# Performance work log

Measured on AMD Instinct MI355X. Metric: run time of the kernel, lower is better.

The kernel has to match this reference:

```python
import jax, jax.numpy as jnp
import numpy as np

T, B, F = 256, 256, 128      # time, batch, features
H, L, K = 384, 3, 10         # hidden_dim, levels, conv_size
C = H // L                   # chunk_size = 128
G = 4 * H + 2 * L            # gate projection width = 1542
S = H // 6                   # scale bottleneck = 64


def setup_inputs() -> dict:
    key = jax.random.key(0)
    ks = jax.random.split(key, 14)
    s = 0.02
    n = lambda k, shp: (jax.random.normal(k, shp, jnp.float32) * s)
    return {
        "x":   jax.random.normal(ks[0], (T, B, F), jnp.float32),
        "Wk":  n(ks[1], (F + 1, G)),   # input kernel (in+interval -> 4H+2L)
        "bk":  jnp.zeros((G,), jnp.float32),
        "Wr":  n(ks[2], (H + 1, G)),   # recurrent kernel
        "br":  jnp.zeros((G,), jnp.float32),
        "Ws":  n(ks[3], (H, S)),       # nn_scale
        "bs":  jnp.zeros((S,), jnp.float32),
        "Wrs": n(ks[4], (S, H)),       # nn_rescale
        "brs": jnp.zeros((H,), jnp.float32),
        "Wc":  n(ks[5], (H, H, K)),    # nn_conv weight (out, in, kernel)
        "bc":  jnp.zeros((H,), jnp.float32),
        "Wo":  n(ks[6], (H, 1)),       # nn_output (n_class==2 -> out_dim 1)
        "bo":  jnp.zeros((1,), jnp.float32),
    }


def _forward(x, Wk, bk, Wr, br, Ws, bs, Wrs, brs, Wc, bc, Wo, bo):
    Bs = x.shape[1]
    ones = jnp.ones((Bs, 1), x.dtype)

    def step(carry, x_t):
        c, h, buf_h, buf_d = carry
        xo = (jnp.concatenate([x_t, ones], -1) @ Wk + bk
              + jnp.concatenate([h, ones], -1) @ Wr + br)       # (B, G)
        # hierarchical master gates (ON-LSTM cumax)
        fm = jnp.cumsum(jax.nn.softmax(xo[:, :L], -1), -1)       # l2r (B,L)
        im = jnp.flip(jnp.cumsum(jax.nn.softmax(
            jnp.flip(xo[:, L:2 * L], -1), -1), -1), -1)          # r2l (B,L)
        g = xo[:, 2 * L:].reshape(Bs, 4 * L, C)
        f_g = jax.nn.sigmoid(g[:, :L])
        i_g = jax.nn.sigmoid(g[:, L:2 * L])
        o_g = jax.nn.sigmoid(g[:, 2 * L:3 * L])
        c_in = jnp.tanh(g[:, 3 * L:])
        c_l = c.reshape(Bs, L, C)
        fm3, im3 = fm[:, :, None], im[:, :, None]
        ov = fm3 * im3
        c_new = ov * (f_g * c_l + i_g * c_in) + (fm3 - ov) * c_l + (im3 - ov) * c_in
        h_new = (o_g * jnp.tanh(c_new)).reshape(Bs, H)
        c_new = c_new.reshape(Bs, H)
        cur_d = 1.0 - jnp.mean(fm, -1)                           # (B,)
        # sliding window buffers (K, B, H) / (K, B)
        buf_h = jnp.concatenate([buf_h[1:], h_new[None]], 0)
        buf_d = jnp.concatenate([buf_d[1:], cur_d[None]], 0)
        local_dis = jax.nn.softmax(jnp.cumsum(buf_d.T, 1), 1)    # (B, K)
        local_h = buf_h.transpose(1, 2, 0) * local_dis[:, None, :]  # (B,H,K)
        theme = jax.nn.sigmoid(
            jax.nn.relu(jnp.mean(local_h, -1) @ Ws + bs) @ Wrs + brs)  # (B,H)
        conv = jnp.einsum('bik,oik->bo', local_h, Wc) + bc      # window conv1d
        loc = theme * conv
        return (c_new, h_new, buf_h, buf_d), (h_new, loc)

    init = (jnp.zeros((Bs, H), x.dtype), jnp.zeros((Bs, H), x.dtype),
            jnp.zeros((K, Bs, H), x.dtype), jnp.zeros((K, Bs), x.dtype))
    _, (h_all, loc_all) = jax.lax.scan(step, init, x)
    # residual add, output head, keep last timestep only (as original)
    rnn_last = loc_all[-1] + h_all[-1]                           # (B, H)
    out = jax.nn.sigmoid(rnn_last @ Wo + bo)                     # (B, 1)
    return out


def reference(x, Wk, bk, Wr, br, Ws, bs, Wrs, brs, Wc, bc, Wo, bo):
    return _forward(x, Wk, bk, Wr, br, Ws, bs, Wrs, brs, Wc, bc, Wo, bo)
```

## Files before the change

kernel.cpp:

```cpp
#include <hip/hip_runtime.h>
#include <hip/hip_bf16.h>
#include <math.h>

#define T_STEPS 256
#define BATCH   256
#define FDIM    128
#define HDIM    384
#define LLEV    3
#define KWIN    10
#define GDIM    1542
#define SDIM    64
#define NPAD    1600
#define KA      512
#define BH      (BATCH*HDIM)

typedef __bf16 bf16x8 __attribute__((ext_vector_type(8)));
typedef float  f32x4  __attribute__((ext_vector_type(4)));

__device__ __forceinline__ float sigmoidf_(float x){ return 1.f/(1.f+__expf(-x)); }

__global__ void init_state(float* __restrict__ hf, float* __restrict__ c, __bf16* __restrict__ hb){
    int i = blockIdx.x*256 + threadIdx.x;
    hf[i] = 0.f; c[i] = 0.f; hb[i] = (__bf16)0.f;
}

__global__ void cast_x(const float* __restrict__ x, __bf16* __restrict__ xb, int n){
    int i = (blockIdx.x*256 + threadIdx.x)*4;
    if (i < n){
        float4 v = *(const float4*)(x+i);
        xb[i+0]=(__bf16)v.x; xb[i+1]=(__bf16)v.y; xb[i+2]=(__bf16)v.z; xb[i+3]=(__bf16)v.w;
    }
}

__global__ void pack_w(const float* __restrict__ Wk, const float* __restrict__ bk,
                       const float* __restrict__ Wr, const float* __restrict__ br,
                       __bf16* __restrict__ Bp, float* __restrict__ cvec){
    int gid = blockIdx.x*256 + threadIdx.x;
    int k8  = gid / NPAD;
    int col = gid - k8*NPAD;
    bool valid = (col < 6) || (col >= 64);
    int g = (col < 6) ? col : (col - 58);
    bf16x8 out;
    #pragma unroll
    for (int j=0;j<8;++j){
        int k = k8*8 + j;
        float v = 0.f;
        if (valid) v = (k < HDIM) ? Wr[k*GDIM + g] : Wk[(k-HDIM)*GDIM + g];
        out[j] = (__bf16)v;
    }
    *(bf16x8*)(Bp + (size_t)gid*8) = out;
    if (k8 == 0){
        float cv = 0.f;
        if (valid) cv = Wk[FDIM*GDIM + g] + bk[g] + Wr[HDIM*GDIM + g] + br[g];
        cvec[col] = cv;
    }
}

__global__ __launch_bounds__(256) void step_gemm(const __bf16* __restrict__ hb, const __bf16* __restrict__ xb,
                                                 const __bf16* __restrict__ Bp, const float* __restrict__ cvec,
                                                 float* __restrict__ xo, int t){
    int wave = threadIdx.x >> 6;
    int lane = threadIdx.x & 63;
    int nblk = blockIdx.x % 25;
    int mblk = blockIdx.x / 25;
    int m0 = mblk*64 + wave*16;
    int n0 = nblk*64;
    int row = m0 + (lane & 15);
    int kh  = (lane >> 4) * 8;
    f32x4 acc[4] = {};
    const __bf16* hrow = hb + (size_t)row*HDIM;
    const __bf16* xrow = xb + ((size_t)t*BATCH + row)*FDIM;
    #pragma unroll
    for (int ks=0; ks<12; ++ks){
        int k = ks*32 + kh;
        bf16x8 a = *(const bf16x8*)(hrow + k);
        const __bf16* bp = Bp + (((size_t)(k>>3))*NPAD + n0 + (lane & 15))*8;
        #pragma unroll
        for (int nt=0; nt<4; ++nt){
            bf16x8 bfrag = *(const bf16x8*)(bp + nt*16*8);
            acc[nt] = __builtin_amdgcn_mfma_f32_16x16x32_bf16(a, bfrag, acc[nt], 0,0,0);
        }
    }
    #pragma unroll
    for (int ks=12; ks<16; ++ks){
        int k = ks*32 + kh;
        bf16x8 a = *(const bf16x8*)(xrow + (k - HDIM));
        const __bf16* bp = Bp + (((size_t)(k>>3))*NPAD + n0 + (lane & 15))*8;
        #pragma unroll
        for (int nt=0; nt<4; ++nt){
            bf16x8 bfrag = *(const bf16x8*)(bp + nt*16*8);
            acc[nt] = __builtin_amdgcn_mfma_f32_16x16x32_bf16(a, bfrag, acc[nt], 0,0,0);
        }
    }
    int r0   = m0 + ((lane >> 4) << 2);
    int ccol = lane & 15;
    #pragma unroll
    for (int nt=0; nt<4; ++nt){
        int col = n0 + nt*16 + ccol;
        float cv = cvec[col];
        #pragma unroll
        for (int i=0;i<4;++i)
            xo[(size_t)(r0+i)*NPAD + col] = acc[nt][i] + cv;
    }
}

__global__ void step_gates(const float* __restrict__ xo, float* __restrict__ c,
                           float* __restrict__ hf, __bf16* __restrict__ hb,
                           float* __restrict__ bufh, float* __restrict__ bufd, int t){
    int gid = blockIdx.x*256 + threadIdx.x;
    int b = gid / HDIM;
    int u = gid - b*HDIM;
    const float* xr = xo + (size_t)b*NPAD;
    float a0=xr[0], a1=xr[1], a2=xr[2];
    float m1 = fmaxf(fmaxf(a0,a1),a2);
    float e0=__expf(a0-m1), e1=__expf(a1-m1), e2=__expf(a2-m1);
    float inv = 1.f/(e0+e1+e2);
    float fm0 = e0*inv, fm1 = fm0 + e1*inv, fm2 = fm1 + e2*inv;
    float b0=xr[3], b1=xr[4], b2=xr[5];
    float m2 = fmaxf(fmaxf(b0,b1),b2);
    float f0=__expf(b0-m2), f1=__expf(b1-m2), f2=__expf(b2-m2);
    float inv2 = 1.f/(f0+f1+f2);
    float im2 = f2*inv2, im1 = im2 + f1*inv2, im0 = im1 + f0*inv2;
    int l = u >> 7;
    float fml = (l==0)?fm0:((l==1)?fm1:fm2);
    float iml = (l==0)?im0:((l==1)?im1:im2);
    float fg = sigmoidf_(xr[64 + u]);
    float ig = sigmoidf_(xr[64 + 384 + u]);
    float og = sigmoidf_(xr[64 + 768 + u]);
    float ci = tanhf   (xr[64 + 1152 + u]);
    float cold = c[gid];
    float ov = fml*iml;
    float cn = ov*(fg*cold + ig*ci) + (fml-ov)*cold + (iml-ov)*ci;
    float h  = og * tanhf(cn);
    c[gid] = cn; hf[gid] = h; hb[gid] = (__bf16)h;
    if (t >= T_STEPS - KWIN){
        int slot = t - (T_STEPS - KWIN);
        bufh[(size_t)slot*BH + gid] = h;
        if (u == 0) bufd[slot*BATCH + b] = 1.f - (fm0+fm1+fm2)*(1.f/3.f);
    }
}

__global__ void final_locdis(const float* __restrict__ bufd, float* __restrict__ locdis){
    int b = threadIdx.x;
    float d[KWIN]; float cum = 0.f;
    #pragma unroll
    for (int k=0;k<KWIN;++k){ cum += bufd[k*BATCH + b]; d[k] = cum; }
    float m = d[0];
    #pragma unroll
    for (int k=1;k<KWIN;++k) m = fmaxf(m, d[k]);
    float s = 0.f;
    #pragma unroll
    for (int k=0;k<KWIN;++k){ d[k] = __expf(d[k]-m); s += d[k]; }
    float invs = 1.f/s;
    #pragma unroll
    for (int k=0;k<KWIN;++k) locdis[b*KWIN + k] = d[k]*invs;
}

__global__ void final_lh(const float* __restrict__ bufh, const float* __restrict__ locdis,
                         float* __restrict__ lh, float* __restrict__ mh){
    int gid = blockIdx.x*256 + threadIdx.x;
    int b = gid / HDIM;
    int i = gid - b*HDIM;
    float s = 0.f;
    #pragma unroll
    for (int k=0;k<KWIN;++k){
        float v = bufh[(size_t)k*BH + gid] * locdis[b*KWIN + k];
        lh[(size_t)b*(HDIM*KWIN) + i*KWIN + k] = v;
        s += v;
    }
    mh[gid] = s * (1.f/KWIN);
}

__global__ __launch_bounds__(256) void final_conv(const float* __restrict__ lh, const float* __restrict__ Wc,
                                                  const float* __restrict__ bc, float* __restrict__ cvout){
    __shared__ float As[32*257];
    __shared__ float Bs[32*257];
    int tid = threadIdx.x;
    int bb = blockIdx.x / 12, ob = blockIdx.x % 12;
    int tx = tid & 15, ty = tid >> 4;
    float acc00=0.f, acc01=0.f, acc10=0.f, acc11=0.f;
    const int KD = HDIM*KWIN;
    for (int ch=0; ch<15; ++ch){
        #pragma unroll
        for (int p=0;p<8;++p){
            int q   = tid + p*256;
            int row = q >> 6;
            int c4  = q & 63;
            float4 va = *(const float4*)(lh + (size_t)(bb*32+row)*KD + ch*256 + c4*4);
            float4 vb = *(const float4*)(Wc + (size_t)(ob*32+row)*KD + ch*256 + c4*4);
            int o = row*257 + c4*4;
            As[o+0]=va.x; As[o+1]=va.y; As[o+2]=va.z; As[o+3]=va.w;
            Bs[o+0]=vb.x; Bs[o+1]=vb.y; Bs[o+2]=vb.z; Bs[o+3]=vb.w;
        }
        __syncthreads();
        for (int kk=0; kk<256; ++kk){
            float x0 = As[ty*257+kk],      x1 = As[(ty+16)*257+kk];
            float w0 = Bs[tx*257+kk],      w1 = Bs[(tx+16)*257+kk];
            acc00 += x0*w0; acc01 += x0*w1; acc10 += x1*w0; acc11 += x1*w1;
        }
        __syncthreads();
    }
    int r0 = bb*32+ty, r1 = r0+16, o0 = ob*32+tx, o1 = o0+16;
    cvout[(size_t)r0*HDIM + o0] = acc00 + bc[o0];
    cvout[(size_t)r0*HDIM + o1] = acc01 + bc[o1];
    cvout[(size_t)r1*HDIM + o0] = acc10 + bc[o0];
    cvout[(size_t)r1*HDIM + o1] = acc11 + bc[o1];
}

__global__ void final_th1(const float* __restrict__ mh, const float* __restrict__ Ws,
                          const float* __restrict__ bs, float* __restrict__ th1){
    int gid = blockIdx.x*256 + threadIdx.x;
    int b = gid >> 6, s = gid & 63;
    float acc = bs[s];
    const float* mr = mh + (size_t)b*HDIM;
    for (int i=0;i<HDIM;++i) acc += mr[i] * Ws[i*SDIM + s];
    th1[gid] = fmaxf(acc, 0.f);
}

__global__ void final_theme(const float* __restrict__ th1, const float* __restrict__ Wrs,
                            const float* __restrict__ brs, float* __restrict__ theme){
    int gid = blockIdx.x*256 + threadIdx.x;
    int b = gid / HDIM, o = gid - b*HDIM;
    float acc = brs[o];
    const float* tr = th1 + b*SDIM;
    for (int j=0;j<SDIM;++j) acc += tr[j] * Wrs[j*HDIM + o];
    theme[gid] = sigmoidf_(acc);
}

__global__ void final_out(const float* __restrict__ theme, const float* __restrict__ cvout,
                          const float* __restrict__ hf, const float* __restrict__ Wo,
                          const float* __restrict__ bo, float* __restrict__ out){
    int b = blockIdx.x, lane = threadIdx.x;
    float s = 0.f;
    for (int u=lane; u<HDIM; u+=64){
        float r = theme[(size_t)b*HDIM+u]*cvout[(size_t)b*HDIM+u] + hf[(size_t)b*HDIM+u];
        s += r * Wo[u];
    }
    #pragma unroll
    for (int off=32; off; off>>=1) s += __shfl_down(s, off);
    if (lane == 0) out[b] = sigmoidf_(s + bo[0]);
}

extern "C" void kernel_launch(void* const* d_in, const int* in_sizes, int n_in,
                              void* d_out, int out_size, void* d_ws, size_t ws_size,
                              hipStream_t stream){
    const float* x   = (const float*)d_in[0];
    const float* Wk  = (const float*)d_in[1];
    const float* bk  = (const float*)d_in[2];
    const float* Wr  = (const float*)d_in[3];
    const float* br  = (const float*)d_in[4];
    const float* Ws  = (const float*)d_in[5];
    const float* bs  = (const float*)d_in[6];
    const float* Wrs = (const float*)d_in[7];
    const float* brs = (const float*)d_in[8];
    const float* Wc  = (const float*)d_in[9];
    const float* bc  = (const float*)d_in[10];
    const float* Wo  = (const float*)d_in[11];
    const float* bo  = (const float*)d_in[12];
    float* out = (float*)d_out;

    char* w = (char*)d_ws;
    auto alloc = [&](size_t bytes)->char*{ char* p = w; w += (bytes + 255) & ~(size_t)255; return p; };
    __bf16* xb    = (__bf16*)alloc((size_t)T_STEPS*BATCH*FDIM*2);
    __bf16* Bp    = (__bf16*)alloc((size_t)(KA/8)*NPAD*8*2);
    float* cvec   = (float*) alloc(NPAD*4);
    float* hf     = (float*) alloc((size_t)BH*4);
    __bf16* hb    = (__bf16*)alloc((size_t)BH*2);
    float* c      = (float*) alloc((size_t)BH*4);
    float* xo     = (float*) alloc((size_t)BATCH*NPAD*4);
    float* bufh   = (float*) alloc((size_t)KWIN*BH*4);
    float* bufd   = (float*) alloc((size_t)KWIN*BATCH*4);
    float* locdis = (float*) alloc((size_t)BATCH*KWIN*4);
    float* lh     = (float*) alloc((size_t)BATCH*HDIM*KWIN*4);
    float* mh     = (float*) alloc((size_t)BH*4);
    float* th1    = (float*) alloc((size_t)BATCH*SDIM*4);
    float* theme  = (float*) alloc((size_t)BH*4);
    float* convb  = (float*) alloc((size_t)BH*4);

    init_state<<<dim3(BH/256), dim3(256), 0, stream>>>(hf, c, hb);
    cast_x<<<dim3((T_STEPS*BATCH*FDIM)/4/256), dim3(256), 0, stream>>>(x, xb, T_STEPS*BATCH*FDIM);
    pack_w<<<dim3((KA/8)*NPAD/256), dim3(256), 0, stream>>>(Wk, bk, Wr, br, Bp, cvec);

    for (int t=0; t<T_STEPS; ++t){
        step_gemm <<<dim3(100), dim3(256), 0, stream>>>(hb, xb, Bp, cvec, xo, t);
        step_gates<<<dim3(BH/256), dim3(256), 0, stream>>>(xo, c, hf, hb, bufh, bufd, t);
    }

    final_locdis<<<dim3(1),   dim3(256), 0, stream>>>(bufd, locdis);
    final_lh    <<<dim3(BH/256), dim3(256), 0, stream>>>(bufh, locdis, lh, mh);
    final_conv  <<<dim3(96),  dim3(256), 0, stream>>>(lh, Wc, bc, convb);
    final_th1   <<<dim3(BATCH*SDIM/256), dim3(256), 0, stream>>>(mh, Ws, bs, th1);
    final_theme <<<dim3(BH/256), dim3(256), 0, stream>>>(th1, Wrs, brs, theme);
    final_out   <<<dim3(BATCH), dim3(64), 0, stream>>>(theme, convb, hf, Wo, bo, out);
}
```

Baseline: 2.410 ms.

## Fuse per-step gate GEMM with LSTM cell update using gate-interleaved weight layout

Merges the per-timestep GEMM and gate-activation kernels into one kernel. The gate weights are repacked so each block's 64 output columns hold the f/i/o/c gates for the same 16 hidden units, and the 6 master-gate columns are computed redundantly by every block through an extra MFMA. The cell update then runs directly from registers, and the hidden state is ping-ponged between two buffers. This removes one launch per step and the global round trip of the xo intermediate, at the cost of duplicated head MFMAs and a block-wide sync.

```diff
diff --git a/kernel.cpp b/kernel.cpp
--- a/kernel.cpp
+++ b/kernel.cpp
@@ -10,7 +10,7 @@
 #define KWIN    10
 #define GDIM    1542
 #define SDIM    64
-#define NPAD    1600
+#define NGC     1536
 #define KA      512
 #define BH      (BATCH*HDIM)
 
@@ -19,9 +19,9 @@
 
 __device__ __forceinline__ float sigmoidf_(float x){ return 1.f/(1.f+__expf(-x)); }
 
-__global__ void init_state(float* __restrict__ hf, float* __restrict__ c, __bf16* __restrict__ hb){
+__global__ void init_state(float* __restrict__ c, __bf16* __restrict__ hbA){
     int i = blockIdx.x*256 + threadIdx.x;
-    hf[i] = 0.f; c[i] = 0.f; hb[i] = (__bf16)0.f;
+    c[i] = 0.f; hbA[i] = (__bf16)0.f;
 }
 
 __global__ void cast_x(const float* __restrict__ x, __bf16* __restrict__ xb, int n){
@@ -32,111 +32,135 @@
     }
 }
 
-__global__ void pack_w(const float* __restrict__ Wk, const float* __restrict__ bk,
-                       const float* __restrict__ Wr, const float* __restrict__ br,
-                       __bf16* __restrict__ Bp, float* __restrict__ cvec){
-    int gid = blockIdx.x*256 + threadIdx.x;
-    int k8  = gid / NPAD;
-    int col = gid - k8*NPAD;
-    bool valid = (col < 6) || (col >= 64);
-    int g = (col < 6) ? col : (col - 58);
+__global__ void pack_w_gate(const float* __restrict__ Wk, const float* __restrict__ bk,
+                            const float* __restrict__ Wr, const float* __restrict__ br,
+                            __bf16* __restrict__ Bg, float* __restrict__ cg){
+    int gid = blockIdx.x*256 + threadIdx.x;
+    int k8  = gid / NGC;
+    int col = gid - k8*NGC;
+    int ugrp = col >> 6;
+    int rem  = col & 63;
+    int gate = rem >> 4;
+    int um   = rem & 15;
+    int u    = ugrp*16 + um;
+    int g    = 6 + gate*HDIM + u;
+    bf16x8 out;
+    #pragma unroll
+    for (int j=0;j<8;++j){
+        int k = k8*8 + j;
+        float v = (k < HDIM) ? Wr[k*GDIM + g] : Wk[(k-HDIM)*GDIM + g];
+        out[j] = (__bf16)v;
+    }
+    *(bf16x8*)(Bg + (size_t)gid*8) = out;
+    if (k8 == 0)
+        cg[col] = Wk[FDIM*GDIM + g] + bk[g] + Wr[HDIM*GDIM + g] + br[g];
+}
+
+__global__ void pack_w_head(const float* __restrict__ Wk, const float* __restrict__ bk,
+                            const float* __restrict__ Wr, const float* __restrict__ br,
+                            __bf16* __restrict__ Bh, float* __restrict__ ch){
+    int gid = blockIdx.x*256 + threadIdx.x;
+    int k8  = gid >> 4;
+    int colh = gid & 15;
     bf16x8 out;
     #pragma unroll
     for (int j=0;j<8;++j){
         int k = k8*8 + j;
         float v = 0.f;
-        if (valid) v = (k < HDIM) ? Wr[k*GDIM + g] : Wk[(k-HDIM)*GDIM + g];
+        if (colh < 6) v = (k < HDIM) ? Wr[k*GDIM + colh] : Wk[(k-HDIM)*GDIM + colh];
         out[j] = (__bf16)v;
     }
-    *(bf16x8*)(Bp + (size_t)gid*8) = out;
-    if (k8 == 0){
-        float cv = 0.f;
-        if (valid) cv = Wk[FDIM*GDIM + g] + bk[g] + Wr[HDIM*GDIM + g] + br[g];
-        cvec[col] = cv;
-    }
-}
-
-__global__ __launch_bounds__(256) void step_gemm(const __bf16* __restrict__ hb, const __bf16* __restrict__ xb,
-                                                 const __bf16* __restrict__ Bp, const float* __restrict__ cvec,
-                                                 float* __restrict__ xo, int t){
-    int wave = threadIdx.x >> 6;
-    int lane = threadIdx.x & 63;
-    int nblk = blockIdx.x % 25;
-    int mblk = blockIdx.x / 25;
-    int m0 = mblk*64 + wave*16;
-    int n0 = nblk*64;
-    int row = m0 + (lane & 15);
-    int kh  = (lane >> 4) * 8;
-    f32x4 acc[4] = {};
-    const __bf16* hrow = hb + (size_t)row*HDIM;
-    const __bf16* xrow = xb + ((size_t)t*BATCH + row)*FDIM;
-    #pragma unroll
-    for (int ks=0; ks<12; ++ks){
+    *(bf16x8*)(Bh + (size_t)gid*8) = out;
+    if (k8 == 0)
+        ch[colh] = (colh < 6) ? (Wk[FDIM*GDIM + colh] + bk[colh] + Wr[HDIM*GDIM + colh] + br[colh]) : 0.f;
+}
+
+__global__ __launch_bounds__(256) void step_fused(
+    const __bf16* __restrict__ hbp, __bf16* __restrict__ hbn,
+    const __bf16* __restrict__ xb,
+    const __bf16* __restrict__ Bg, const __bf16* __restrict__ Bh,
+    const float* __restrict__ cg, const float* __restrict__ ch,
+    float* __restrict__ c, float* __restrict__ hf,
+    float* __restrict__ bufh, float* __restrict__ bufd, int t)
+{
+    __shared__ float headlds[4][16][8];
+    int tid  = threadIdx.x;
+    int wave = tid >> 6, lane = tid & 63;
+    int mblk = blockIdx.x / 24, ublk = blockIdx.x % 24;
+    int m0   = mblk*64 + wave*16;
+    int ccol = lane & 15;
+    int krow = lane >> 4;
+    int arow = m0 + ccol;
+    int kh   = krow*8;
+
+    f32x4 acc[4] = {}; f32x4 acch = {};
+    const __bf16* hrow   = hbp + (size_t)arow*HDIM;
+    const __bf16* xrow   = xb + ((size_t)t*BATCH + arow)*FDIM;
+    const __bf16* bgbase = Bg + ((size_t)ublk*64 + ccol)*8;
+    const __bf16* bhbase = Bh + (size_t)ccol*8;
+
+    #pragma unroll
+    for (int ks=0; ks<16; ++ks){
         int k = ks*32 + kh;
-        bf16x8 a = *(const bf16x8*)(hrow + k);
-        const __bf16* bp = Bp + (((size_t)(k>>3))*NPAD + n0 + (lane & 15))*8;
+        bf16x8 a = (ks < 12) ? *(const bf16x8*)(hrow + k)
+                             : *(const bf16x8*)(xrow + (k - HDIM));
+        const __bf16* bp = bgbase + (size_t)(k>>3)*NGC*8;
         #pragma unroll
         for (int nt=0; nt<4; ++nt){
             bf16x8 bfrag = *(const bf16x8*)(bp + nt*16*8);
             acc[nt] = __builtin_amdgcn_mfma_f32_16x16x32_bf16(a, bfrag, acc[nt], 0,0,0);
         }
-    }
-    #pragma unroll
-    for (int ks=12; ks<16; ++ks){
-        int k = ks*32 + kh;
-        bf16x8 a = *(const bf16x8*)(xrow + (k - HDIM));
-        const __bf16* bp = Bp + (((size_t)(k>>3))*NPAD + n0 + (lane & 15))*8;
-        #pragma unroll
-        for (int nt=0; nt<4; ++nt){
-            bf16x8 bfrag = *(const bf16x8*)(bp + nt*16*8);
-            acc[nt] = __builtin_amdgcn_mfma_f32_16x16x32_bf16(a, bfrag, acc[nt], 0,0,0);
-        }
-    }
-    int r0   = m0 + ((lane >> 4) << 2);
-    int ccol = lane & 15;
-    #pragma unroll
-    for (int nt=0; nt<4; ++nt){
-        int col = n0 + nt*16 + ccol;
-        float cv = cvec[col];
+        bf16x8 bh = *(const bf16x8*)(bhbase + (size_t)(k>>3)*16*8);
+        acch = __builtin_amdgcn_mfma_f32_16x16x32_bf16(a, bh, acch, 0,0,0);
+    }
+
+    if (ccol < 6){
+        float cv = ch[ccol];
         #pragma unroll
         for (int i=0;i<4;++i)
-            xo[(size_t)(r0+i)*NPAD + col] = acc[nt][i] + cv;
-    }
-}
-
-__global__ void step_gates(const float* __restrict__ xo, float* __restrict__ c,
-                           float* __restrict__ hf, __bf16* __restrict__ hb,
-                           float* __restrict__ bufh, float* __restrict__ bufd, int t){
-    int gid = blockIdx.x*256 + threadIdx.x;
-    int b = gid / HDIM;
-    int u = gid - b*HDIM;
-    const float* xr = xo + (size_t)b*NPAD;
-    float a0=xr[0], a1=xr[1], a2=xr[2];
-    float m1 = fmaxf(fmaxf(a0,a1),a2);
-    float e0=__expf(a0-m1), e1=__expf(a1-m1), e2=__expf(a2-m1);
-    float inv = 1.f/(e0+e1+e2);
-    float fm0 = e0*inv, fm1 = fm0 + e1*inv, fm2 = fm1 + e2*inv;
-    float b0=xr[3], b1=xr[4], b2=xr[5];
-    float m2 = fmaxf(fmaxf(b0,b1),b2);
-    float f0=__expf(b0-m2), f1=__expf(b1-m2), f2=__expf(b2-m2);
-    float inv2 = 1.f/(f0+f1+f2);
-    float im2 = f2*inv2, im1 = im2 + f1*inv2, im0 = im1 + f0*inv2;
+            headlds[wave][krow*4+i][ccol] = acch[i] + cv;
+    }
+    __syncthreads();
+
+    int u = ublk*16 + ccol;
     int l = u >> 7;
-    float fml = (l==0)?fm0:((l==1)?fm1:fm2);
-    float iml = (l==0)?im0:((l==1)?im1:im2);
-    float fg = sigmoidf_(xr[64 + u]);
-    float ig = sigmoidf_(xr[64 + 384 + u]);
-    float og = sigmoidf_(xr[64 + 768 + u]);
-    float ci = tanhf   (xr[64 + 1152 + u]);
-    float cold = c[gid];
-    float ov = fml*iml;
-    float cn = ov*(fg*cold + ig*ci) + (fml-ov)*cold + (iml-ov)*ci;
-    float h  = og * tanhf(cn);
-    c[gid] = cn; hf[gid] = h; hb[gid] = (__bf16)h;
-    if (t >= T_STEPS - KWIN){
-        int slot = t - (T_STEPS - KWIN);
-        bufh[(size_t)slot*BH + gid] = h;
-        if (u == 0) bufd[slot*BATCH + b] = 1.f - (fm0+fm1+fm2)*(1.f/3.f);
+    float cgv0 = cg[ublk*64 +  0 + ccol];
+    float cgv1 = cg[ublk*64 + 16 + ccol];
+    float cgv2 = cg[ublk*64 + 32 + ccol];
+    float cgv3 = cg[ublk*64 + 48 + ccol];
+    int slot = t - (T_STEPS - KWIN);
+
+    #pragma unroll
+    for (int i=0;i<4;++i){
+        int rl = krow*4 + i;
+        int R  = m0 + rl;
+        float a0 = headlds[wave][rl][0], a1 = headlds[wave][rl][1], a2 = headlds[wave][rl][2];
+        float b0 = headlds[wave][rl][3], b1 = headlds[wave][rl][4], b2 = headlds[wave][rl][5];
+        float m1v = fmaxf(fmaxf(a0,a1),a2);
+        float e0=__expf(a0-m1v), e1=__expf(a1-m1v), e2=__expf(a2-m1v);
+        float inv = 1.f/(e0+e1+e2);
+        float fm0 = e0*inv, fm1 = fm0 + e1*inv, fm2 = fm1 + e2*inv;
+        float m2v = fmaxf(fmaxf(b0,b1),b2);
+        float f0=__expf(b0-m2v), f1=__expf(b1-m2v), f2=__expf(b2-m2v);
+        float inv2 = 1.f/(f0+f1+f2);
+        float im2 = f2*inv2, im1 = im2 + f1*inv2, im0 = im1 + f0*inv2;
+        float fml = (l==0)?fm0:((l==1)?fm1:fm2);
+        float iml = (l==0)?im0:((l==1)?im1:im2);
+        float fg = sigmoidf_(acc[0][i] + cgv0);
+        float ig = sigmoidf_(acc[1][i] + cgv1);
+        float og = sigmoidf_(acc[2][i] + cgv2);
+        float ci = tanhf   (acc[3][i] + cgv3);
+        size_t idx = (size_t)R*HDIM + u;
+        float cold = c[idx];
+        float ov = fml*iml;
+        float cn = ov*(fg*cold + ig*ci) + (fml-ov)*cold + (iml-ov)*ci;
+        float h  = og * tanhf(cn);
+        c[idx] = cn;
+        hbn[idx] = (__bf16)h;
+        if (slot >= 0) bufh[(size_t)slot*BH + idx] = h;
+        if (t == T_STEPS-1) hf[idx] = h;
+        if (slot >= 0 && ublk == 0 && ccol == 0)
+            bufd[slot*BATCH + R] = 1.f - (fm0+fm1+fm2)*(1.f/3.f);
     }
 }
 
@@ -262,12 +286,14 @@
     char* w = (char*)d_ws;
     auto alloc = [&](size_t bytes)->char*{ char* p = w; w += (bytes + 255) & ~(size_t)255; return p; };
     __bf16* xb    = (__bf16*)alloc((size_t)T_STEPS*BATCH*FDIM*2);
-    __bf16* Bp    = (__bf16*)alloc((size_t)(KA/8)*NPAD*8*2);
-    float* cvec   = (float*) alloc(NPAD*4);
+    __bf16* Bg    = (__bf16*)alloc((size_t)(KA/8)*NGC*8*2);
+    __bf16* Bh    = (__bf16*)alloc((size_t)(KA/8)*16*8*2);
+    float* cg     = (float*) alloc(NGC*4);
+    float* ch     = (float*) alloc(16*4);
+    __bf16* hbA   = (__bf16*)alloc((size_t)BH*2);
+    __bf16* hbB   = (__bf16*)alloc((size_t)BH*2);
     float* hf     = (float*) alloc((size_t)BH*4);
-    __bf16* hb    = (__bf16*)alloc((size_t)BH*2);
     float* c      = (float*) alloc((size_t)BH*4);
-    float* xo     = (float*) alloc((size_t)BATCH*NPAD*4);
     float* bufh   = (float*) alloc((size_t)KWIN*BH*4);
     float* bufd   = (float*) alloc((size_t)KWIN*BATCH*4);
     float* locdis = (float*) alloc((size_t)BATCH*KWIN*4);
@@ -277,13 +303,16 @@
     float* theme  = (float*) alloc((size_t)BH*4);
     float* convb  = (float*) alloc((size_t)BH*4);
 
-    init_state<<<dim3(BH/256), dim3(256), 0, stream>>>(hf, c, hb);
+    init_state<<<dim3(BH/256), dim3(256), 0, stream>>>(c, hbA);
     cast_x<<<dim3((T_STEPS*BATCH*FDIM)/4/256), dim3(256), 0, stream>>>(x, xb, T_STEPS*BATCH*FDIM);
-    pack_w<<<dim3((KA/8)*NPAD/256), dim3(256), 0, stream>>>(Wk, bk, Wr, br, Bp, cvec);
+    pack_w_gate<<<dim3((KA/8)*NGC/256), dim3(256), 0, stream>>>(Wk, bk, Wr, br, Bg, cg);
+    pack_w_head<<<dim3((KA/8)*16/256), dim3(256), 0, stream>>>(Wk, bk, Wr, br, Bh, ch);
 
     for (int t=0; t<T_STEPS; ++t){
-        step_gemm <<<dim3(100), dim3(256), 0, stream>>>(hb, xb, Bp, cvec, xo, t);
-        step_gates<<<dim3(BH/256), dim3(256), 0, stream>>>(xo, c, hf, hb, bufh, bufd, t);
+        const __bf16* hp = (t & 1) ? hbB : hbA;
+        __bf16*       hn = (t & 1) ? hbA : hbB;
+        step_fused<<<dim3(96), dim3(256), 0, stream>>>(hp, hn, xb, Bg, Bh, cg, ch,
+                                                       c, hf, bufh, bufd, t);
     }
 
     final_locdis<<<dim3(1),   dim3(256), 0, stream>>>(bufd, locdis);
```

Measured after the change: 2.913 ms. 20.9% more time.
